# Performance work log

Measured on AMD Instinct MI355X. Metric: run time of the kernel, lower is better.

## Reference

```python
import jax, jax.numpy as jnp
import numpy as np
import math

B, S, DIM = 1, 2048, 4096
N_HEADS, N_KV, HEAD_DIM = 32, 8, 128
WINDOW = 2048
ROPE_THETA = 10000.0


def setup_inputs() -> dict:
    key = jax.random.key(0)
    ks = jax.random.split(key, 6)
    w_std = 0.02
    x = jax.random.normal(ks[0], (B, S, DIM), dtype=jnp.float32)
    wq = jax.random.normal(ks[1], (DIM, N_HEADS * HEAD_DIM), dtype=jnp.float32) * w_std
    wk = jax.random.normal(ks[2], (DIM, N_KV * HEAD_DIM), dtype=jnp.float32) * w_std
    wv = jax.random.normal(ks[3], (DIM, N_KV * HEAD_DIM), dtype=jnp.float32) * w_std
    wo = jax.random.normal(ks[4], (N_HEADS * HEAD_DIM, DIM), dtype=jnp.float32) * w_std
    # rotary tables (real/imag of complex_rotary_matrix)
    pos = jnp.arange(S, dtype=jnp.float32)
    inv_freq = 1.0 / (ROPE_THETA ** (jnp.arange(0, HEAD_DIM, 2, dtype=jnp.float32) / HEAD_DIM))
    angles = pos[:, None] * inv_freq[None, :]  # [S, HEAD_DIM/2]
    cos, sin = jnp.cos(angles), jnp.sin(angles)
    positions = jnp.arange(S, dtype=jnp.int32)
    # sliding-window causal additive mask: allow j <= i and i - j < WINDOW
    i = jnp.arange(S)[:, None]
    j = jnp.arange(S)[None, :]
    allowed = (j <= i) & (i - j < WINDOW)
    mask = jnp.where(allowed, 0.0, -jnp.inf).astype(jnp.float32)
    cache_k = jnp.zeros((B, WINDOW, N_KV, HEAD_DIM), dtype=jnp.float32)
    cache_v = jnp.zeros((B, WINDOW, N_KV, HEAD_DIM), dtype=jnp.float32)
    return dict(x=x, wq=wq, wk=wk, wv=wv, wo=wo, cos=cos, sin=sin,
                positions=positions, mask=mask, cache_k=cache_k, cache_v=cache_v)


def _apply_rope(t, cos, sin):
    # t: [B, S, H, D]; interleaved complex pairs as in torch.view_as_complex
    tp = t.reshape(*t.shape[:-1], HEAD_DIM // 2, 2)
    te, to = tp[..., 0], tp[..., 1]
    c = cos[None, :, None, :]
    s = sin[None, :, None, :]
    re = te * c - to * s
    im = te * s + to * c
    return jnp.stack([re, im], axis=-1).reshape(t.shape)


def reference(x, wq, wk, wv, wo, cos, sin, positions, mask, cache_k, cache_v):
    repeats = N_HEADS // N_KV
    q = (x @ wq).reshape(B, S, N_HEADS, HEAD_DIM)
    k = (x @ wk).reshape(B, S, N_KV, HEAD_DIM)
    v = (x @ wv).reshape(B, S, N_KV, HEAD_DIM)
    q = _apply_rope(q, cos, sin)
    k = _apply_rope(k, cos, sin)
    # rolling KV-cache scatter update (prefill path: positions.shape[0] > 1)
    scatter_pos = positions[-WINDOW:] % WINDOW
    new_cache_k = cache_k.at[:, scatter_pos].set(k[:, -WINDOW:])
    new_cache_v = cache_v.at[:, scatter_pos].set(v[:, -WINDOW:])
    # GQA head repetition (repeat_kv_head)
    k = jnp.repeat(k, repeats, axis=2)  # [B, S, N_HEADS, D]
    v = jnp.repeat(v, repeats, axis=2)
    scores = jnp.einsum('bqhd,bkhd->bhqk', q, k) / math.sqrt(HEAD_DIM)
    scores = scores + mask[None, None, :, :]
    attn = jax.nn.softmax(scores.astype(jnp.float32), axis=-1).astype(q.dtype)
    out = jnp.einsum('bhqk,bkhd->bqhd', attn, v)
    out = out.reshape(B, S, N_HEADS * HEAD_DIM)
    return out @ wo, new_cache_k, new_cache_v
```

## Files before the change

kernel.cpp:

```cpp
#include <hip/hip_runtime.h>

typedef __bf16 bf16;
typedef __bf16 bf16x8 __attribute__((ext_vector_type(8)));
typedef __bf16 bf16x4 __attribute__((ext_vector_type(4)));
typedef float  f32x4  __attribute__((ext_vector_type(4)));

__device__ __forceinline__ f32x4 mfma16(bf16x8 a, bf16x8 b, f32x4 c) {
  return __builtin_amdgcn_mfma_f32_16x16x32_bf16(a, b, c, 0, 0, 0);
}

__device__ __forceinline__ void gload16(const bf16* g, bf16* l) {
  __builtin_amdgcn_global_load_lds(
      (const __attribute__((address_space(1))) void*)g,
      (__attribute__((address_space(3))) void*)l, 16, 0, 0);
}

__global__ void cast_x_kernel(const float* __restrict__ in, bf16* __restrict__ out) {
  const int i = blockIdx.x * 256 + threadIdx.x;
  const float4 v = ((const float4*)in)[i];
  bf16x4 o;
  o[0] = (bf16)v.x; o[1] = (bf16)v.y; o[2] = (bf16)v.z; o[3] = (bf16)v.w;
  *(bf16x4*)&out[(size_t)i * 4] = o;
}

__global__ void transpose_cast64(const float* __restrict__ in, bf16* __restrict__ out,
                                 int ldin, int ldout) {
  __shared__ bf16 t[64][68];
  const int c0 = blockIdx.x * 64, r0 = blockIdx.y * 64;
  const int g4 = threadIdx.x & 15;
  const int q  = threadIdx.x >> 4;
  #pragma unroll
  for (int i = 0; i < 4; ++i) {
    const int r = q + i * 16;
    const float4 v = *(const float4*)&in[(size_t)(r0 + r) * ldin + c0 + g4 * 4];
    bf16x4 b;
    b[0] = (bf16)v.x; b[1] = (bf16)v.y; b[2] = (bf16)v.z; b[3] = (bf16)v.w;
    *(bf16x4*)&t[r][g4 * 4] = b;
  }
  __syncthreads();
  #pragma unroll
  for (int i = 0; i < 4; ++i) {
    const int c = q + i * 16;
    bf16x4 b;
    b[0] = t[g4 * 4 + 0][c]; b[1] = t[g4 * 4 + 1][c];
    b[2] = t[g4 * 4 + 2][c]; b[3] = t[g4 * 4 + 3][c];
    *(bf16x4*)&out[(size_t)(c0 + c) * ldout + r0 + g4 * 4] = b;
  }
}

__global__ void permute_v(const bf16* __restrict__ qkv, bf16* __restrict__ vp,
                          float* __restrict__ cv) {
  __shared__ bf16 t[32][33];
  const int sb  = blockIdx.x;
  const int kvh = blockIdx.y >> 2;
  const int dt  = blockIdx.y & 3;
  const int x = threadIdx.x, y = threadIdx.y;
  #pragma unroll
  for (int i = 0; i < 32; i += 8) {
    const bf16 v = qkv[(size_t)(sb * 32 + y + i) * 6144 + 5120 + kvh * 128 + dt * 32 + x];
    t[y + i][x] = v;
    cv[(size_t)(sb * 32 + y + i) * 1024 + kvh * 128 + dt * 32 + x] = (float)v;
  }
  __syncthreads();
  #pragma unroll
  for (int i = 0; i < 32; i += 8)
    vp[((size_t)(kvh * 64 + sb) * 128 + dt * 32 + y + i) * 32 + x] = t[x][y + i];
}

#define MMQ(MB, NB)                                                            \
  _Pragma("unroll")                                                            \
  for (int mi = 0; mi < 4; ++mi)                                               \
    _Pragma("unroll")                                                          \
    for (int ni = 0; ni < 2; ++ni)                                             \
      _Pragma("unroll")                                                        \
      for (int kk = 0; kk < 2; ++kk)                                           \
        acc[MB + mi][NB + ni] =                                                \
            mfma16(ar[mi][kk], br[NB + ni][kk], acc[MB + mi][NB + ni]);

#define PH_OPEN                                                                \
  __builtin_amdgcn_s_barrier();                                                \
  asm volatile("s_waitcnt lgkmcnt(0)" ::: "memory");                           \
  __builtin_amdgcn_s_setprio(1);

#define PH_CLOSE                                                               \
  __builtin_amdgcn_s_setprio(0);                                               \
  __builtin_amdgcn_s_barrier();

template <typename OutT, int NSPLIT>
__global__ __launch_bounds__(512, 2)
void gemm8(const bf16* __restrict__ A, const bf16* __restrict__ Bt,
           OutT* __restrict__ C0, OutT* __restrict__ C1,
           int M, int N, int K, int ldc) {
  __shared__ __attribute__((aligned(16))) bf16 lds[65536];
  char* ldsc = (char*)lds;
  constexpr int AO0 = 0, BO0 = 32768, AO1 = 65536, BO1 = 98304;

  const int t    = threadIdx.x;
  const int w    = t >> 6;
  const int lane = t & 63;
  const int l15  = lane & 15;
  const int lg   = lane >> 4;
  const int wm   = w >> 2;
  const int wn   = w & 3;
  const int hb   = wn >> 1;

  const int nbm = M >> 8;
  const int nb2 = nbm * NSPLIT;
  const int cpx = (nb2 * (N >> 8)) >> 3;
  const int lid = ((int)blockIdx.x & 7) * cpx + ((int)blockIdx.x >> 3);
  const int bn  = (lid / nb2) * 256;
  const int rem = lid % nb2;
  const int kh  = rem / nbm;
  const int bm  = (rem % nbm) * 256;
  const int Kloc = K / NSPLIT;
  const int koff = kh * Kloc;
  OutT* __restrict__ C = (NSPLIT == 2 && kh) ? C1 : C0;

  const int d0     = t * 16;
  const int dsw    = d0 ^ (((d0 >> 9) & 1) << 5);
  const int srow_s = (dsw >> 6) & 127;
  const int scol_e = (dsw & 63) >> 1;

  auto stg = [&](const bf16* P, int rowbase, int tile, int half, int region) {
    const bf16* s = P + (size_t)(rowbase + half * 128 + srow_s) * K +
                    koff + tile * 64 + scol_e;
    gload16(s,      (bf16*)(ldsc + region + half * 16384 + w * 1024));
    gload16(s + 32, (bf16*)(ldsc + region + half * 16384 + 8192 + w * 1024));
  };
  auto lda = [&](int AO, int m, int kk) -> bf16x8 {
    int byte = AO + wm * 16384 + kk * 8192 + (m * 16 + l15) * 64 + lg * 16;
    byte ^= ((byte >> 9) & 1) << 5;
    return *(const bf16x8*)(ldsc + byte);
  };
  auto ldb = [&](int BO, int n, int kk) -> bf16x8 {
    int byte = BO + hb * 16384 + kk * 8192 +
               ((wn & 1) * 64 + n * 16 + l15) * 64 + lg * 16;
    byte ^= ((byte >> 9) & 1) << 5;
    return *(const bf16x8*)(ldsc + byte);
  };

  f32x4 acc[8][4] = {};
  bf16x8 ar[4][2], br[4][2];

  const int NT = Kloc >> 6;
  const int NI = Kloc >> 7;

  stg(A,  bm, 0, 0, AO0);  stg(A,  bm, 0, 1, AO0);
  stg(Bt, bn, 0, 0, BO0);  stg(Bt, bn, 0, 1, BO0);
  stg(Bt, bn, 1, 0, BO1);  stg(Bt, bn, 1, 1, BO1);
  asm volatile("s_waitcnt vmcnt(4)" ::: "memory");
  __builtin_amdgcn_s_barrier();

  #pragma unroll 1
  for (int it = 0; it < NI; ++it) {
    const int t1 = 2 * it + 1;
    const int t2 = (2 * it + 2 < NT) ? 2 * it + 2 : NT - 1;
    const int t3 = (2 * it + 3 < NT) ? 2 * it + 3 : NT - 1;

    #pragma unroll
    for (int mi = 0; mi < 4; ++mi) {
      ar[mi][0] = lda(AO0, mi, 0); ar[mi][1] = lda(AO0, mi, 1);
    }
    #pragma unroll
    for (int ni = 0; ni < 2; ++ni) {
      br[ni][0] = ldb(BO0, ni, 0); br[ni][1] = ldb(BO0, ni, 1);
    }
    stg(A, bm, t1, 0, AO1);
    PH_OPEN; MMQ(0, 0); PH_CLOSE;
    #pragma unroll
    for (int ni = 2; ni < 4; ++ni) {
      br[ni][0] = ldb(BO0, ni, 0); br[ni][1] = ldb(BO0, ni, 1);
    }
    stg(A, bm, t1, 1, AO1);
    PH_OPEN; MMQ(0, 2); PH_CLOSE;
    #pragma unroll
    for (int mi = 0; mi < 4; ++mi) {
      ar[mi][0] = lda(AO0, 4 + mi, 0); ar[mi][1] = lda(AO0, 4 + mi, 1);
    }
    stg(Bt, bn, t2, 0, BO0);
    PH_OPEN; MMQ(4, 0); PH_CLOSE;
    stg(Bt, bn, t2, 1, BO0);
    PH_OPEN; MMQ(4, 2);
    __builtin_amdgcn_s_setprio(0);
    asm volatile("s_waitcnt vmcnt(4)" ::: "memory");
    __builtin_amdgcn_s_barrier();
    #pragma unroll
    for (int mi = 0; mi < 4; ++mi) {
      ar[mi][0] = lda(AO1, mi, 0); ar[mi][1] = lda(AO1, mi, 1);
    }
    #pragma unroll
    for (int ni = 0; ni < 2; ++ni) {
      br[ni][0] = ldb(BO1, ni, 0); br[ni][1] = ldb(BO1, ni, 1);
    }
    stg(A, bm, t2, 0, AO0);
    PH_OPEN; MMQ(0, 0); PH_CLOSE;
    #pragma unroll
    for (int ni = 2; ni < 4; ++ni) {
      br[ni][0] = ldb(BO1, ni, 0); br[ni][1] = ldb(BO1, ni, 1);
    }
    stg(A, bm, t2, 1, AO0);
    PH_OPEN; MMQ(0, 2); PH_CLOSE;
    #pragma unroll
    for (int mi = 0; mi < 4; ++mi) {
      ar[mi][0] = lda(AO1, 4 + mi, 0); ar[mi][1] = lda(AO1, 4 + mi, 1);
    }
    stg(Bt, bn, t3, 0, BO1);
    PH_OPEN; MMQ(4, 0); PH_CLOSE;
    stg(Bt, bn, t3, 1, BO1);
    PH_OPEN; MMQ(4, 2);
    __builtin_amdgcn_s_setprio(0);
    asm volatile("s_waitcnt vmcnt(4)" ::: "memory");
    __builtin_amdgcn_s_barrier();
  }

  #pragma unroll
  for (int mi = 0; mi < 8; ++mi)
    #pragma unroll
    for (int ni = 0; ni < 4; ++ni)
      #pragma unroll
      for (int rr = 0; rr < 4; ++rr)
        C[(size_t)(bm + wm * 128 + mi * 16 + lg * 4 + rr) * ldc +
          (bn + wn * 64 + ni * 16 + l15)] = (OutT)acc[mi][ni][rr];
}

__global__ void reduce_out(const bf16* __restrict__ p0, const bf16* __restrict__ p1,
                           float* __restrict__ out) {
  const int i = blockIdx.x * 256 + threadIdx.x;
  const bf16x4 a = *(const bf16x4*)&p0[(size_t)i * 4];
  const bf16x4 b = *(const bf16x4*)&p1[(size_t)i * 4];
  float4 o;
  o.x = (float)a[0] + (float)b[0];
  o.y = (float)a[1] + (float)b[1];
  o.z = (float)a[2] + (float)b[2];
  o.w = (float)a[3] + (float)b[3];
  *(float4*)&out[(size_t)i * 4] = o;
}

__global__ void rope_q_kernel(bf16* __restrict__ q, const float* __restrict__ cs,
                              const float* __restrict__ sn) {
  const int idx = blockIdx.x * 256 + threadIdx.x;
  const int p  = idx & 63;
  const int sh = idx >> 6;
  const int h  = sh & 31;
  const int s  = sh >> 5;
  const float c  = cs[s * 64 + p];
  const float si = sn[s * 64 + p];
  const size_t ii = (size_t)s * 6144 + h * 128 + 2 * p;
  const float te = (float)q[ii], to = (float)q[ii + 1];
  q[ii]     = (bf16)(te * c - to * si);
  q[ii + 1] = (bf16)(te * si + to * c);
}

__global__ void rope_k_kernel(const bf16* __restrict__ qkv, bf16* __restrict__ kp,
                              float* __restrict__ ck, const float* __restrict__ cs,
                              const float* __restrict__ sn) {
  const int idx = blockIdx.x * 256 + threadIdx.x;
  const int p  = idx & 63;
  const int sh = idx >> 6;
  const int h  = sh & 7;
  const int s  = sh >> 3;
  const float c  = cs[s * 64 + p];
  const float si = sn[s * 64 + p];
  const size_t ii = (size_t)s * 6144 + 4096 + h * 128 + 2 * p;
  const float te = (float)qkv[ii], to = (float)qkv[ii + 1];
  const float re = te * c - to * si;
  const float im = te * si + to * c;
  const size_t io = ((size_t)(h * 4 + (p >> 4)) * 2048 + s) * 32 + ((2 * p) & 31);
  kp[io]     = (bf16)re;
  kp[io + 1] = (bf16)im;
  const size_t ic = (size_t)s * 1024 + h * 128 + 2 * p;
  ck[ic]     = re;
  ck[ic + 1] = im;
}

__global__ __launch_bounds__(256, 3)
void attn_fwd(const bf16* __restrict__ Q, const bf16* __restrict__ Kp,
              const bf16* __restrict__ Vp, bf16* __restrict__ O) {
  __shared__ __attribute__((aligned(16))) bf16 Kb[8192];
  __shared__ __attribute__((aligned(16))) bf16 Vb[8192];
  __shared__ __attribute__((aligned(16))) bf16 P_lds[4][16][72];
  const int id   = blockIdx.x;
  const int qt   = 31 - (id >> 5);
  const int kvh  = id & 7;
  const int sub  = (id >> 3) & 3;
  const int h    = kvh * 4 + sub;
  const int t    = threadIdx.x;
  const int w    = t >> 6;
  const int lane = t & 63;
  const int l15  = lane & 15;
  const int lg   = lane >> 4;
  const float scale = 0.08838834764831845f;
  const bf16* Kh = Kp + (size_t)kvh * 262144;
  const bf16* Vh = Vp + (size_t)kvh * 262144;
  const int koff = (t >> 2) * 32 + (t & 3) * 8;

  const int qw  = qt * 64 + w * 16;
  const int myq = qw + l15;

  bf16x8 qf[4];
  #pragma unroll
  for (int ds = 0; ds < 4; ++ds)
    qf[ds] = *(const bf16x8*)&Q[(size_t)myq * 6144 + h * 128 + ds * 32 + lg * 8];

  f32x4 o[8] = {};
  float m = -1e30f, ell = 0.f;

  #pragma unroll
  for (int i = 0; i < 4; ++i)
    gload16(Kh + (size_t)i * 65536 + koff, Kb + i * 2048 + w * 512);
  #pragma unroll
  for (int i = 0; i < 4; ++i)
    gload16(Vh + (size_t)i * 2048 + koff, Vb + i * 2048 + w * 512);
  __syncthreads();

  #pragma unroll 1
  for (int kt = 0; kt <= qt; ++kt) {
    f32x4 T[4] = {};
    __builtin_amdgcn_s_setprio(1);
    #pragma unroll
    for (int kb = 0; kb < 4; ++kb)
      #pragma unroll
      for (int ds = 0; ds < 4; ++ds) {
        bf16x8 kf = *(const bf16x8*)&Kb[(ds * 64 + kb * 16 + l15) * 32 + lg * 8];
        T[kb] = mfma16(kf, qf[ds], T[kb]);
      }
    __builtin_amdgcn_s_setprio(0);
    __syncthreads();
    if (kt < qt) {
      #pragma unroll
      for (int i = 0; i < 4; ++i)
        gload16(Kh + (size_t)i * 65536 + (kt + 1) * 2048 + koff,
                Kb + i * 2048 + w * 512);
    }

    float pv[16];
    float pmax = -1e30f;
    if (kt == qt) {
      #pragma unroll
      for (int kb = 0; kb < 4; ++kb)
        #pragma unroll
        for (int r = 0; r < 4; ++r) {
          const int key = qt * 64 + kb * 16 + lg * 4 + r;
          const float s = (key > myq) ? -1e30f : T[kb][r] * scale;
          pv[kb * 4 + r] = s;
          pmax = fmaxf(pmax, s);
        }
    } else {
      #pragma unroll
      for (int kb = 0; kb < 4; ++kb)
        #pragma unroll
        for (int r = 0; r < 4; ++r) {
          const float s = T[kb][r] * scale;
          pv[kb * 4 + r] = s;
          pmax = fmaxf(pmax, s);
        }
    }
    float base = m;
    if (!__all(pmax - m <= 8.f)) {
      float wmax = pmax;
      wmax = fmaxf(wmax, __shfl_xor(wmax, 16));
      wmax = fmaxf(wmax, __shfl_xor(wmax, 32));
      const float newm = fmaxf(m, wmax);
      const float corr = __expf(m - newm);
      ell *= corr;
      m = newm; base = newm;
      float sf[4];
      #pragma unroll
      for (int r = 0; r < 4; ++r) sf[r] = __shfl(corr, lg * 4 + r);
      #pragma unroll
      for (int df = 0; df < 8; ++df)
        #pragma unroll
        for (int r = 0; r < 4; ++r) o[df][r] *= sf[r];
    }
    bf16 pb[16];
    float tsum = 0.f;
    #pragma unroll
    for (int i = 0; i < 16; ++i) {
      const float p = __expf(pv[i] - base);
      tsum += p;
      pb[i] = (bf16)p;
    }
    ell += tsum;

    #pragma unroll
    for (int kb = 0; kb < 4; ++kb) {
      bf16x4 pk;
      pk[0] = pb[kb * 4 + 0]; pk[1] = pb[kb * 4 + 1];
      pk[2] = pb[kb * 4 + 2]; pk[3] = pb[kb * 4 + 3];
      *(bf16x4*)&P_lds[w][l15][kb * 16 + lg * 4] = pk;
    }
    __builtin_amdgcn_s_setprio(1);
    #pragma unroll
    for (int ks = 0; ks < 2; ++ks) {
      bf16x8 pa = *(const bf16x8*)&P_lds[w][l15][ks * 32 + lg * 8];
      #pragma unroll
      for (int df = 0; df < 8; ++df) {
        bf16x8 vf = *(const bf16x8*)&Vb[(ks * 128 + df * 16 + l15) * 32 + lg * 8];
        o[df] = mfma16(pa, vf, o[df]);
      }
    }
    __builtin_amdgcn_s_setprio(0);
    __syncthreads();
    if (kt < qt) {
      #pragma unroll
      for (int i = 0; i < 4; ++i)
        gload16(Vh + (size_t)(kt + 1) * 8192 + i * 2048 + koff,
                Vb + i * 2048 + w * 512);
    }
  }

  ell += __shfl_xor(ell, 16);
  ell += __shfl_xor(ell, 32);
  float er[4];
  #pragma unroll
  for (int r = 0; r < 4; ++r) er[r] = 1.f / __shfl(ell, lg * 4 + r);
  #pragma unroll
  for (int df = 0; df < 8; ++df)
    #pragma unroll
    for (int r = 0; r < 4; ++r)
      O[(size_t)(qw + lg * 4 + r) * 4096 + h * 128 + df * 16 + l15] =
          (bf16)(o[df][r] * er[r]);
}

extern "C" void kernel_launch(void* const* d_in, const int* in_sizes, int n_in,
                              void* d_out, int out_size, void* d_ws, size_t ws_size,
                              hipStream_t stream) {
  const float* x    = (const float*)d_in[0];
  const float* wq   = (const float*)d_in[1];
  const float* wk   = (const float*)d_in[2];
  const float* wv   = (const float*)d_in[3];
  const float* wo   = (const float*)d_in[4];
  const float* cosf_ = (const float*)d_in[5];
  const float* sinf_ = (const float*)d_in[6];

  float* out     = (float*)d_out;
  float* cache_k = out + (size_t)8388608;
  float* cache_v = cache_k + (size_t)2097152;
  bf16* qkv = (bf16*)d_out;

  bf16* ws = (bf16*)d_ws;
  bf16* wT = ws;
  bf16* kp = ws + (size_t)25165824;
  bf16* vp = kp + (size_t)2097152;
  bf16* xb = vp + (size_t)2097152;
  bf16* aout = xb;
  bf16* part1 = wT + (size_t)16777216;
  bf16* part0 = ws + (size_t)37748736;

  cast_x_kernel<<<8192, 256, 0, stream>>>(x, xb);
  transpose_cast64<<<dim3(64, 64), 256, 0, stream>>>(wq, wT, 4096, 4096);
  transpose_cast64<<<dim3(16, 64), 256, 0, stream>>>(wk, wT + (size_t)16777216,
                                                     1024, 4096);
  transpose_cast64<<<dim3(16, 64), 256, 0, stream>>>(wv, wT + (size_t)20971520,
                                                     1024, 4096);
  gemm8<bf16, 1><<<192, 512, 0, stream>>>(xb, wT, qkv, qkv, 2048, 6144, 4096, 6144);
  rope_q_kernel<<<16384, 256, 0, stream>>>(qkv, cosf_, sinf_);
  rope_k_kernel<<<4096, 256, 0, stream>>>(qkv, kp, cache_k, cosf_, sinf_);
  permute_v<<<dim3(64, 32), dim3(32, 8), 0, stream>>>(qkv, vp, cache_v);
  transpose_cast64<<<dim3(64, 64), 256, 0, stream>>>(wo, wT, 4096, 4096);
  attn_fwd<<<1024, 256, 0, stream>>>(qkv, kp, vp, aout);
  gemm8<bf16, 2><<<256, 512, 0, stream>>>(aout, wT, part0, part1,
                                          2048, 4096, 4096, 4096);
  reduce_out<<<8192, 256, 0, stream>>>(part0, part1, out);
}
```

Baseline: 322.6 us.

## Share K/V tiles across two GQA heads per attention block

The attention kernel now runs 512-thread blocks in which eight waves cover two query heads that share the same KV head, and the grid is halved. Each K/V tile staged in LDS is reused by both heads, so global traffic for K and V is halved and each thread issues half as many async loads. In exchange, blocks are larger and occupancy drops (launch bounds 512,2), so there are fewer blocks in flight for latency hiding and causal load balancing.

```diff
diff --git a/kernel.cpp b/kernel.cpp
--- a/kernel.cpp
+++ b/kernel.cpp
@@ -273,28 +273,29 @@
   ck[ic + 1] = im;
 }
 
-__global__ __launch_bounds__(256, 3)
+__global__ __launch_bounds__(512, 2)
 void attn_fwd(const bf16* __restrict__ Q, const bf16* __restrict__ Kp,
               const bf16* __restrict__ Vp, bf16* __restrict__ O) {
   __shared__ __attribute__((aligned(16))) bf16 Kb[8192];
   __shared__ __attribute__((aligned(16))) bf16 Vb[8192];
-  __shared__ __attribute__((aligned(16))) bf16 P_lds[4][16][72];
+  __shared__ __attribute__((aligned(16))) bf16 P_lds[8][16][72];
   const int id   = blockIdx.x;
-  const int qt   = 31 - (id >> 5);
+  const int qt   = 31 - (id >> 4);
   const int kvh  = id & 7;
-  const int sub  = (id >> 3) & 3;
-  const int h    = kvh * 4 + sub;
+  const int sub  = (id >> 3) & 1;
   const int t    = threadIdx.x;
   const int w    = t >> 6;
+  const int wi   = w & 3;
+  const int h    = kvh * 4 + sub * 2 + (w >> 2);
   const int lane = t & 63;
   const int l15  = lane & 15;
   const int lg   = lane >> 4;
   const float scale = 0.08838834764831845f;
   const bf16* Kh = Kp + (size_t)kvh * 262144;
   const bf16* Vh = Vp + (size_t)kvh * 262144;
-  const int koff = (t >> 2) * 32 + (t & 3) * 8;
-
-  const int qw  = qt * 64 + w * 16;
+  const int lsub = ((t & 63) >> 2) * 32 + (t & 3) * 8;
+
+  const int qw  = qt * 64 + wi * 16;
   const int myq = qw + l15;
 
   bf16x8 qf[4];
@@ -306,11 +307,16 @@
   float m = -1e30f, ell = 0.f;
 
   #pragma unroll
-  for (int i = 0; i < 4; ++i)
-    gload16(Kh + (size_t)i * 65536 + koff, Kb + i * 2048 + w * 512);
-  #pragma unroll
-  for (int i = 0; i < 4; ++i)
-    gload16(Vh + (size_t)i * 2048 + koff, Vb + i * 2048 + w * 512);
+  for (int i = 0; i < 2; ++i) {
+    const int c = i * 8 + w;
+    gload16(Kh + (size_t)(c >> 2) * 65536 + (size_t)((c & 3) * 16) * 32 + lsub,
+            Kb + c * 512);
+  }
+  #pragma unroll
+  for (int i = 0; i < 2; ++i) {
+    const int c = i * 8 + w;
+    gload16(Vh + (size_t)c * 512 + lsub, Vb + c * 512);
+  }
   __syncthreads();
 
   #pragma unroll 1
@@ -328,9 +334,12 @@
     __syncthreads();
     if (kt < qt) {
       #pragma unroll
-      for (int i = 0; i < 4; ++i)
-        gload16(Kh + (size_t)i * 65536 + (kt + 1) * 2048 + koff,
-                Kb + i * 2048 + w * 512);
+      for (int i = 0; i < 2; ++i) {
+        const int c = i * 8 + w;
+        gload16(Kh + (size_t)(c >> 2) * 65536 +
+                    (size_t)((kt + 1) * 64 + (c & 3) * 16) * 32 + lsub,
+                Kb + c * 512);
+      }
     }
 
     float pv[16];
@@ -403,9 +412,10 @@
     __syncthreads();
     if (kt < qt) {
       #pragma unroll
-      for (int i = 0; i < 4; ++i)
-        gload16(Vh + (size_t)(kt + 1) * 8192 + i * 2048 + koff,
-                Vb + i * 2048 + w * 512);
+      for (int i = 0; i < 2; ++i) {
+        const int c = i * 8 + w;
+        gload16(Vh + (size_t)(kt + 1) * 8192 + c * 512 + lsub, Vb + c * 512);
+      }
     }
   }
 
@@ -458,7 +468,7 @@
   rope_k_kernel<<<4096, 256, 0, stream>>>(qkv, kp, cache_k, cosf_, sinf_);
   permute_v<<<dim3(64, 32), dim3(32, 8), 0, stream>>>(qkv, vp, cache_v);
   transpose_cast64<<<dim3(64, 64), 256, 0, stream>>>(wo, wT, 4096, 4096);
-  attn_fwd<<<1024, 256, 0, stream>>>(qkv, kp, vp, aout);
+  attn_fwd<<<512, 512, 0, stream>>>(qkv, kp, vp, aout);
   gemm8<bf16, 2><<<256, 512, 0, stream>>>(aout, wT, part0, part1,
                                           2048, 4096, 4096, 4096);
   reduce_out<<<8192, 256, 0, stream>>>(part0, part1, out);
```

Result: slower. 330.1 us (+2.3%).

## Use 256x192 GEMM tile for QKV projection to fill all CUs

Applied to the files above, without the earlier changes.

Adds a gemm8n192 kernel variant with a 256x192 output tile (each wave computes 128x48). It replaces the 256x256-tile QKV GEMM, which launched 192 blocks, with a 256-block launch. The goal is better CU occupancy and wave balance on the 256-CU MI355X. The cost is a smaller N tile, which means less reuse of the A operand per block and a reworked LDS staging and phase schedule.

```diff
diff --git a/kernel.cpp b/kernel.cpp
--- a/kernel.cpp
+++ b/kernel.cpp
@@ -76,6 +76,13 @@
       for (int kk = 0; kk < 2; ++kk)                                           \
         acc[MB + mi][NB + ni] =                                                \
             mfma16(ar[mi][kk], br[NB + ni][kk], acc[MB + mi][NB + ni]);
+
+#define MMQ1(MB)                                                               \
+  _Pragma("unroll")                                                            \
+  for (int mi = 0; mi < 4; ++mi)                                               \
+    _Pragma("unroll")                                                          \
+    for (int kk = 0; kk < 2; ++kk)                                             \
+      acc[MB + mi][2] = mfma16(ar[mi][kk], br[2][kk], acc[MB + mi][2]);
 
 #define PH_OPEN                                                                \
   __builtin_amdgcn_s_barrier();                                                \
@@ -221,6 +228,133 @@
       for (int rr = 0; rr < 4; ++rr)
         C[(size_t)(bm + wm * 128 + mi * 16 + lg * 4 + rr) * ldc +
           (bn + wn * 64 + ni * 16 + l15)] = (OutT)acc[mi][ni][rr];
+}
+
+__global__ __launch_bounds__(512, 2)
+void gemm8n192(const bf16* __restrict__ A, const bf16* __restrict__ Bt,
+               bf16* __restrict__ C, int M, int N, int K, int ldc) {
+  __shared__ __attribute__((aligned(16))) bf16 lds[57344];
+  char* ldsc = (char*)lds;
+  constexpr int AO0 = 0, BO0 = 32768, AO1 = 57344, BO1 = 90112;
+
+  const int t    = threadIdx.x;
+  const int w    = t >> 6;
+  const int lane = t & 63;
+  const int l15  = lane & 15;
+  const int lg   = lane >> 4;
+  const int wm   = w >> 2;
+  const int wn   = w & 3;
+
+  const int cpx = 32;
+  const int lid = ((int)blockIdx.x & 7) * cpx + ((int)blockIdx.x >> 3);
+  const int bn  = (lid >> 3) * 192;
+  const int bm  = (lid & 7) * 256;
+
+  const int d0     = t * 16;
+  const int dsw    = d0 ^ (((d0 >> 9) & 1) << 5);
+  const int srow_a = (dsw >> 6) & 127;
+  const int scol_e = (dsw & 63) >> 1;
+  const int rw_b   = (t >> 2) & 63;
+  const int kk_b   = t >> 8;
+
+  auto stga = [&](int tile, int half, int region) {
+    const bf16* s = A + (size_t)(bm + half * 128 + srow_a) * K + tile * 64 + scol_e;
+    gload16(s,      (bf16*)(ldsc + region + half * 16384 + w * 1024));
+    gload16(s + 32, (bf16*)(ldsc + region + half * 16384 + 8192 + w * 1024));
+  };
+  auto stgb = [&](int tile, int third, int region) {
+    const bf16* s = Bt + (size_t)(bn + third * 64 + rw_b) * K +
+                    tile * 64 + kk_b * 32 + scol_e;
+    gload16(s, (bf16*)(ldsc + region + third * 8192 + w * 1024));
+  };
+  auto lda = [&](int AO, int m, int kk) -> bf16x8 {
+    int byte = AO + wm * 16384 + kk * 8192 + (m * 16 + l15) * 64 + lg * 16;
+    byte ^= ((byte >> 9) & 1) << 5;
+    return *(const bf16x8*)(ldsc + byte);
+  };
+  auto ldb = [&](int BO, int n, int kk) -> bf16x8 {
+    const int row = wn * 48 + n * 16 + l15;
+    int byte = BO + (row >> 6) * 8192 + kk * 4096 + (row & 63) * 64 + lg * 16;
+    byte ^= ((byte >> 9) & 1) << 5;
+    return *(const bf16x8*)(ldsc + byte);
+  };
+
+  f32x4 acc[8][3] = {};
+  bf16x8 ar[4][2], br[3][2];
+
+  const int NT = K >> 6;
+  const int NI = K >> 7;
+
+  stga(0, 0, AO0); stga(0, 1, AO0);
+  stgb(0, 0, BO0); stgb(0, 1, BO0); stgb(0, 2, BO0);
+  stgb(1, 0, BO1); stgb(1, 1, BO1); stgb(1, 2, BO1);
+  asm volatile("s_waitcnt vmcnt(3)" ::: "memory");
+  __builtin_amdgcn_s_barrier();
+
+  #pragma unroll 1
+  for (int it = 0; it < NI; ++it) {
+    const int t1 = 2 * it + 1;
+    const int t2 = (2 * it + 2 < NT) ? 2 * it + 2 : NT - 1;
+    const int t3 = (2 * it + 3 < NT) ? 2 * it + 3 : NT - 1;
+
+    #pragma unroll
+    for (int mi = 0; mi < 4; ++mi) {
+      ar[mi][0] = lda(AO0, mi, 0); ar[mi][1] = lda(AO0, mi, 1);
+    }
+    #pragma unroll
+    for (int ni = 0; ni < 2; ++ni) {
+      br[ni][0] = ldb(BO0, ni, 0); br[ni][1] = ldb(BO0, ni, 1);
+    }
+    stga(t1, 0, AO1);
+    PH_OPEN; MMQ(0, 0); PH_CLOSE;
+    br[2][0] = ldb(BO0, 2, 0); br[2][1] = ldb(BO0, 2, 1);
+    stga(t1, 1, AO1);
+    PH_OPEN; MMQ1(0); PH_CLOSE;
+    #pragma unroll
+    for (int mi = 0; mi < 4; ++mi) {
+      ar[mi][0] = lda(AO0, 4 + mi, 0); ar[mi][1] = lda(AO0, 4 + mi, 1);
+    }
+    stgb(t2, 0, BO0); stgb(t2, 1, BO0);
+    PH_OPEN; MMQ(4, 0); PH_CLOSE;
+    stgb(t2, 2, BO0);
+    PH_OPEN; MMQ1(4);
+    __builtin_amdgcn_s_setprio(0);
+    asm volatile("s_waitcnt vmcnt(3)" ::: "memory");
+    __builtin_amdgcn_s_barrier();
+    #pragma unroll
+    for (int mi = 0; mi < 4; ++mi) {
+      ar[mi][0] = lda(AO1, mi, 0); ar[mi][1] = lda(AO1, mi, 1);
+    }
+    #pragma unroll
+    for (int ni = 0; ni < 2; ++ni) {
+      br[ni][0] = ldb(BO1, ni, 0); br[ni][1] = ldb(BO1, ni, 1);
+    }
+    stga(t2, 0, AO0);
+    PH_OPEN; MMQ(0, 0); PH_CLOSE;
+    br[2][0] = ldb(BO1, 2, 0); br[2][1] = ldb(BO1, 2, 1);
+    stga(t2, 1, AO0);
+    PH_OPEN; MMQ1(0); PH_CLOSE;
+    #pragma unroll
+    for (int mi = 0; mi < 4; ++mi) {
+      ar[mi][0] = lda(AO1, 4 + mi, 0); ar[mi][1] = lda(AO1, 4 + mi, 1);
+    }
+    stgb(t3, 0, BO1); stgb(t3, 1, BO1);
+    PH_OPEN; MMQ(4, 0); PH_CLOSE;
+    stgb(t3, 2, BO1);
+    PH_OPEN; MMQ1(4);
+    __builtin_amdgcn_s_setprio(0);
+    asm volatile("s_waitcnt vmcnt(3)" ::: "memory");
+    __builtin_amdgcn_s_barrier();
+  }
+
+  #pragma unroll
+  for (int mi = 0; mi < 8; ++mi)
+    #pragma unroll
+    for (int ni = 0; ni < 3; ++ni)
+      #pragma unroll
+      for (int rr = 0; rr < 4; ++rr)
+        C[(size_t)(bm + wm * 128 + mi * 16 + lg * 4 + rr) * ldc +
+          (bn + wn * 48 + ni * 16 + l15)] = (bf16)acc[mi][ni][rr];
 }
 
 __global__ void reduce_out(const bf16* __restrict__ p0, const bf16* __restrict__ p1,
@@ -453,7 +587,7 @@
                                                      1024, 4096);
   transpose_cast64<<<dim3(16, 64), 256, 0, stream>>>(wv, wT + (size_t)20971520,
                                                      1024, 4096);
-  gemm8<bf16, 1><<<192, 512, 0, stream>>>(xb, wT, qkv, qkv, 2048, 6144, 4096, 6144);
+  gemm8n192<<<256, 512, 0, stream>>>(xb, wT, qkv, 2048, 6144, 4096, 6144);
   rope_q_kernel<<<16384, 256, 0, stream>>>(qkv, cosf_, sinf_);
   rope_k_kernel<<<4096, 256, 0, stream>>>(qkv, kp, cache_k, cosf_, sinf_);
   permute_v<<<dim3(64, 32), dim3(32, 8), 0, stream>>>(qkv, vp, cache_v);
```

Result: faster. 303.7 us (-5.9%).
